# Performance work log

Measured on AMD Instinct MI355X. Metric: run time of the kernel, lower is better.

## Reference

```python
import jax, jax.numpy as jnp
import numpy as np

B, C, T, H = 64, 64, 2048, 128  # batch, input channels, time steps, hidden_dim


def setup_inputs() -> dict:
    key = jax.random.key(0)
    ks = jax.random.split(key, 14)
    s = 0.05
    d = {
        'x': jax.random.normal(ks[0], (B, C, T), jnp.float32),
        # forward-direction LSTM params (PyTorch gate order i,f,g,o)
        'Wih_f': jax.random.normal(ks[1], (4 * H, C), jnp.float32) * s,
        'Whh_f': jax.random.normal(ks[2], (4 * H, H), jnp.float32) * s,
        'bih_f': jax.random.normal(ks[3], (4 * H,), jnp.float32) * s,
        'bhh_f': jax.random.normal(ks[4], (4 * H,), jnp.float32) * s,
        # backward-direction LSTM params
        'Wih_b': jax.random.normal(ks[5], (4 * H, C), jnp.float32) * s,
        'Whh_b': jax.random.normal(ks[6], (4 * H, H), jnp.float32) * s,
        'bih_b': jax.random.normal(ks[7], (4 * H,), jnp.float32) * s,
        'bhh_b': jax.random.normal(ks[8], (4 * H,), jnp.float32) * s,
        # attention params
        'Wa': jax.random.normal(ks[9], (2 * H, 2 * H), jnp.float32) * s,
        'ba': jax.random.normal(ks[10], (2 * H,), jnp.float32) * s,
        'Wu': jax.random.normal(ks[11], (1, 2 * H), jnp.float32) * s,
        'bu': jax.random.normal(ks[12], (1,), jnp.float32) * s,
    }
    return d


def _lstm_dir(xt, Wih, Whh, bih, bhh):
    # xt: (B, T, C) -> hs: (B, T, H). PyTorch gate order: i, f, g, o.
    Bb, Tt, _ = xt.shape
    Hh = Whh.shape[1]
    z_in = jnp.einsum('btc,gc->btg', xt, Wih) + bih + bhh  # (B, T, 4H)

    def step(carry, z_t):
        h, c = carry
        z = z_t + h @ Whh.T
        i, f, g, o = jnp.split(z, 4, axis=-1)
        c = jax.nn.sigmoid(f) * c + jax.nn.sigmoid(i) * jnp.tanh(g)
        h = jax.nn.sigmoid(o) * jnp.tanh(c)
        return (h, c), h

    h0 = jnp.zeros((Bb, Hh), xt.dtype)
    _, hs = jax.lax.scan(step, (h0, h0), jnp.swapaxes(z_in, 0, 1))
    return jnp.swapaxes(hs, 0, 1)


def reference(x, Wih_f, Whh_f, bih_f, bhh_f, Wih_b, Whh_b, bih_b, bhh_b, Wa, ba, Wu, bu):
    xt = jnp.swapaxes(x, 1, 2)                       # (B, T, C)
    h_fwd = _lstm_dir(xt, Wih_f, Whh_f, bih_f, bhh_f)
    h_bwd = _lstm_dir(xt[:, ::-1], Wih_b, Whh_b, bih_b, bhh_b)[:, ::-1]
    lstm_out = jnp.concatenate([h_fwd, h_bwd], axis=-1)  # (B, T, 2H)
    u = jnp.tanh(jnp.einsum('bth,gh->btg', lstm_out, Wa) + ba)
    scores = jnp.einsum('btg,og->bto', u, Wu)[..., 0] + bu[0]  # (B, T)
    w = jax.nn.softmax(scores, axis=1)
    attended = jnp.einsum('bth,bt->bh', lstm_out, w)  # (B, 2H)
    return attended
```

## Files before the change

kernel.cpp:

```cpp
#include <hip/hip_runtime.h>
#include <hip/hip_bf16.h>
#include <cstdint>

#define Bb 64
#define Cc 64
#define Tt 2048
#define Hh 128
#define RING 18
#define HRS 1024
#define XPS 524

typedef __fp16 h2    __attribute__((ext_vector_type(2)));
typedef __fp16 f16x8 __attribute__((ext_vector_type(8)));
typedef float  f32x4 __attribute__((ext_vector_type(4)));

union P8 { uint4 u; f16x8 v; h2 p[4]; __fp16 h[8]; };
union P2 { unsigned int u; h2 p; };

#if __has_builtin(__builtin_amdgcn_exp2f)
#define EXP2F(v) __builtin_amdgcn_exp2f(v)
#else
#define EXP2F(v) __expf(0.69314718056f * (v))
#endif
#define RCPF(v) __builtin_amdgcn_rcpf(v)
#define L2E 1.44269504089f

__device__ __forceinline__ float ftanh(float xx) {
    return 1.0f - 2.0f / (__expf(2.0f * xx) + 1.0f);
}

__device__ __forceinline__ f16x8 cvt8s(float4 a, float4 b, float s) {
    P8 u;
    u.p[0] = __builtin_amdgcn_cvt_pkrtz(a.x * s, a.y * s);
    u.p[1] = __builtin_amdgcn_cvt_pkrtz(a.z * s, a.w * s);
    u.p[2] = __builtin_amdgcn_cvt_pkrtz(b.x * s, b.y * s);
    u.p[3] = __builtin_amdgcn_cvt_pkrtz(b.z * s, b.w * s);
    return u.v;
}

__global__ __launch_bounds__(512, 2) void lstm_kernel(
    const float* __restrict__ x,
    const float* __restrict__ Wih_f, const float* __restrict__ Whh_f,
    const float* __restrict__ bih_f, const float* __restrict__ bhh_f,
    const float* __restrict__ Wih_b, const float* __restrict__ Whh_b,
    const float* __restrict__ bih_b, const float* __restrict__ bhh_b,
    __fp16* __restrict__ y)
{
    const int blk = blockIdx.x;
    const int dir = blk >> 2;
    const int bg  = blk & 3;
    const int tid = threadIdx.x;
    const int w   = tid >> 6;
    const int l   = tid & 63;
    const int col = l & 15;
    const int hi  = l >> 4;

    const float* Wih = dir ? Wih_b : Wih_f;
    const float* Whh = dir ? Whh_b : Whh_f;
    const float* bih = dir ? bih_b : bih_f;
    const float* bhh = dir ? bhh_b : bhh_f;

    f16x8 whA[4][4];
    f16x8 wxA[4][2];
    float bias[4][4];
    float cst[4] = {0.0f, 0.0f, 0.0f, 0.0f};
    #pragma unroll
    for (int m = 0; m < 4; ++m) {
        const float s = (m == 2) ? (2.0f * L2E) : L2E;
        const int rowA = (m << 7) + (w << 4) + col;
        #pragma unroll
        for (int kk = 0; kk < 4; ++kk) {
            const float* p = Whh + (size_t)rowA * 128 + kk * 32 + hi * 8;
            whA[m][kk] = cvt8s(*(const float4*)p, *(const float4*)(p + 4), s);
        }
        #pragma unroll
        for (int kk = 0; kk < 2; ++kk) {
            const float* p = Wih + (size_t)rowA * 64 + kk * 32 + hi * 8;
            wxA[m][kk] = cvt8s(*(const float4*)p, *(const float4*)(p + 4), s);
        }
        #pragma unroll
        for (int r = 0; r < 4; ++r) {
            const int rowC = (m << 7) + (w << 4) + (hi << 2) + r;
            bias[m][r] = (bih[rowC] + bhh[rowC]) * s;
        }
    }

    __shared__ __align__(16) unsigned int lds_hr[RING * HRS];
    __shared__ __align__(16) unsigned int lds_xs[16 * XPS];

    for (int i = tid; i < HRS; i += 512) lds_hr[(RING - 1) * HRS + i] = 0u;

    const int gsw = ((hi << 4) + (col ^ hi)) << 2;
    const int hiw = ((w & 1) << 1) + (hi >> 1);
    const int wgsw = ((w >> 1) << 8) + (((hiw << 4) + (col ^ hiw)) << 2) + ((hi & 1) << 1);

    const size_t xbase = (size_t)(bg * 16) * Cc * Tt;
    int slp = RING - 1;
    int slc = 0;

    #pragma unroll 1
    for (int tile = 0; tile < Tt / 16; ++tile) {
        const int s0  = tile << 4;
        const int sl0 = slc;

        #pragma unroll
        for (int it = 0; it < 4; ++it) {
            int i = tid + (it << 9);
            int tq = i & 3, cp = (i >> 2) & 31, b = i >> 7;
            int tb = dir ? (Tt - 4 - s0 - (tq << 2)) : (s0 + (tq << 2));
            const float* rA = x + xbase + ((size_t)b * Cc + 2 * cp) * Tt + tb;
            float4 va = *(const float4*)rA;
            float4 vb = *(const float4*)(rA + Tt);
            const float* pa = (const float*)&va;
            const float* pb = (const float*)&vb;
            int kk = cp >> 4, hip = (cp >> 2) & 3, e2 = cp & 3;
            int gdst = (kk << 8) + (((hip << 4) + (b ^ hip)) << 2) + e2;
            #pragma unroll
            for (int e = 0; e < 4; ++e) {
                int ss = dir ? ((tq << 2) + 3 - e) : ((tq << 2) + e);
                P2 pk; pk.p = __builtin_amdgcn_cvt_pkrtz(pa[e], pb[e]);
                lds_xs[ss * XPS + gdst] = pk.u;
            }
        }
        __syncthreads();

        #pragma unroll 1
        for (int ss = 0; ss < 16; ++ss) {
            const unsigned int* hbase = lds_hr + slp * HRS;
            const unsigned int* xbase2 = lds_xs + ss * XPS;
            P8 hB[4], xB[2];
            #pragma unroll
            for (int kk = 0; kk < 4; ++kk)
                hB[kk].u = *(const uint4*)(hbase + (kk << 8) + gsw);
            #pragma unroll
            for (int kk = 0; kk < 2; ++kk)
                xB[kk].u = *(const uint4*)(xbase2 + (kk << 8) + gsw);

            f32x4 acc[4];
            #pragma unroll
            for (int m = 0; m < 4; ++m) {
                f32x4 a = {0.0f, 0.0f, 0.0f, 0.0f};
                #pragma unroll
                for (int kk = 0; kk < 4; ++kk)
                    a = __builtin_amdgcn_mfma_f32_16x16x32_f16(whA[m][kk], hB[kk].v, a, 0, 0, 0);
                #pragma unroll
                for (int kk = 0; kk < 2; ++kk)
                    a = __builtin_amdgcn_mfma_f32_16x16x32_f16(wxA[m][kk], xB[kk].v, a, 0, 0, 0);
                acc[m] = a;
            }

            float hhv[4];
            #pragma unroll
            for (int r = 0; r < 4; ++r) {
                float zi = acc[0][r] + bias[0][r];
                float zf = acc[1][r] + bias[1][r];
                float zg = acc[2][r] + bias[2][r];
                float zo = acc[3][r] + bias[3][r];
                float si = RCPF(1.0f + EXP2F(-zi));
                float sf = RCPF(1.0f + EXP2F(-zf));
                float so = RCPF(1.0f + EXP2F(-zo));
                float tg = fmaf(-2.0f, RCPF(1.0f + EXP2F(zg)), 1.0f);
                float c  = fmaf(sf, cst[r], si * tg);
                cst[r] = c;
                float tc = fmaf(-2.0f, RCPF(1.0f + EXP2F(2.0f * L2E * c)), 1.0f);
                hhv[r] = so * tc;
            }
            P2 hp0, hp1;
            hp0.p = __builtin_amdgcn_cvt_pkrtz(hhv[0], hhv[1]);
            hp1.p = __builtin_amdgcn_cvt_pkrtz(hhv[2], hhv[3]);
            uint2 wv; wv.x = hp0.u; wv.y = hp1.u;
            *(uint2*)(lds_hr + slc * HRS + wgsw) = wv;
            __syncthreads();
            slp = slc;
            slc = (slc + 1 == RING) ? 0 : slc + 1;
        }

        #pragma unroll
        for (int it = 0; it < 8; ++it) {
            int idx = (it << 3) + w;
            int ssf = idx >> 2, kkf = idx & 3;
            int sl = sl0 + ssf; if (sl >= RING) sl -= RING;
            uint4 v = *(const uint4*)(lds_hr + sl * HRS + (kkf << 8) + (l << 2));
            int bf = (l & 15) ^ (l >> 4);
            int j8 = (kkf << 2) + (l >> 4);
            int t = dir ? (Tt - 1 - (s0 + ssf)) : (s0 + ssf);
            *(uint4*)(y + (((size_t)(bg * 16 + bf) * Tt + t) << 8) + dir * 128 + (j8 << 3)) = v;
        }
    }
}

__global__ __launch_bounds__(512, 2) void attn_scores_kernel(
    const __fp16* __restrict__ y,
    const float* __restrict__ Wa, const float* __restrict__ ba,
    const float* __restrict__ Wu, const float* __restrict__ bu,
    float* __restrict__ scores)
{
    const int b   = blockIdx.y;
    const int t0  = blockIdx.x * 64;
    const int tid = threadIdx.x;
    const int w   = tid >> 6, l = tid & 63;
    const int col = l & 15, hi = l >> 4;

    __shared__ __fp16 y_lds[64][264];
    __shared__ float red[8][64];

    f16x8 wB[2][8];
    float bav[2], wuv[2];
    #pragma unroll
    for (int ns = 0; ns < 2; ++ns) {
        const int g = (w << 5) + (ns << 4) + col;
        #pragma unroll
        for (int kk = 0; kk < 8; ++kk) {
            const float* p = Wa + (size_t)g * 256 + kk * 32 + hi * 8;
            wB[ns][kk] = cvt8s(*(const float4*)p, *(const float4*)(p + 4), 1.0f);
        }
        bav[ns] = ba[g];
        wuv[ns] = Wu[g];
    }

    #pragma unroll
    for (int it = 0; it < 4; ++it) {
        int i = tid + it * 512;
        int tt = i >> 5, c8 = i & 31;
        uint4 v = *(const uint4*)(y + ((size_t)b * Tt + t0 + tt) * 256 + c8 * 8);
        *(uint4*)&y_lds[tt][c8 * 8] = v;
    }
    __syncthreads();

    f32x4 acc[4][2];
    #pragma unroll
    for (int ms = 0; ms < 4; ++ms)
        #pragma unroll
        for (int ns = 0; ns < 2; ++ns) {
            acc[ms][ns][0] = bav[ns]; acc[ms][ns][1] = bav[ns];
            acc[ms][ns][2] = bav[ns]; acc[ms][ns][3] = bav[ns];
        }

    #pragma unroll
    for (int ms = 0; ms < 4; ++ms) {
        #pragma unroll
        for (int kk = 0; kk < 8; ++kk) {
            P8 a;
            a.u = *(const uint4*)&y_lds[(ms << 4) + col][kk * 32 + hi * 8];
            acc[ms][0] = __builtin_amdgcn_mfma_f32_16x16x32_f16(a.v, wB[0][kk], acc[ms][0], 0, 0, 0);
            acc[ms][1] = __builtin_amdgcn_mfma_f32_16x16x32_f16(a.v, wB[1][kk], acc[ms][1], 0, 0, 0);
        }
    }

    #pragma unroll
    for (int ms = 0; ms < 4; ++ms) {
        float pr[4];
        #pragma unroll
        for (int r = 0; r < 4; ++r) {
            pr[r] = wuv[0] * ftanh(acc[ms][0][r]) + wuv[1] * ftanh(acc[ms][1][r]);
            pr[r] += __shfl_xor(pr[r], 1, 64);
            pr[r] += __shfl_xor(pr[r], 2, 64);
            pr[r] += __shfl_xor(pr[r], 4, 64);
            pr[r] += __shfl_xor(pr[r], 8, 64);
        }
        if (col == 0) {
            #pragma unroll
            for (int r = 0; r < 4; ++r)
                red[w][(ms << 4) + (hi << 2) + r] = pr[r];
        }
    }
    __syncthreads();
    if (tid < 64) {
        float ssum = bu[0];
        #pragma unroll
        for (int wv = 0; wv < 8; ++wv) ssum += red[wv][tid];
        scores[(size_t)b * Tt + t0 + tid] = ssum;
    }
}

__global__ __launch_bounds__(256) void attn_out_kernel(
    const __fp16* __restrict__ y,
    const float* __restrict__ scores,
    float* __restrict__ out)
{
    const int b = blockIdx.x;
    const int tid = threadIdx.x;
    const int lane = tid & 63, wid = tid >> 6;
    __shared__ float wls[2048];
    __shared__ float red[4];

    float m = -1e30f;
    for (int t = tid; t < Tt; t += 256) m = fmaxf(m, scores[(size_t)b * Tt + t]);
    #pragma unroll
    for (int off = 32; off >= 1; off >>= 1) m = fmaxf(m, __shfl_xor(m, off, 64));
    if (lane == 0) red[wid] = m;
    __syncthreads();
    m = fmaxf(fmaxf(red[0], red[1]), fmaxf(red[2], red[3]));
    __syncthreads();

    float sum = 0.0f;
    for (int t = tid; t < Tt; t += 256) {
        float e = __expf(scores[(size_t)b * Tt + t] - m);
        wls[t] = e;
        sum += e;
    }
    #pragma unroll
    for (int off = 32; off >= 1; off >>= 1) sum += __shfl_xor(sum, off, 64);
    if (lane == 0) red[wid] = sum;
    __syncthreads();
    const float inv = 1.0f / (red[0] + red[1] + red[2] + red[3]);

    const __fp16* yb = y + (size_t)b * Tt * 256 + tid;
    float acc = 0.0f;
    for (int t = 0; t < Tt; ++t) {
        acc += wls[t] * (float)yb[(size_t)t * 256];
    }
    out[b * 256 + tid] = acc * inv;
}

extern "C" void kernel_launch(void* const* d_in, const int* in_sizes, int n_in,
                              void* d_out, int out_size, void* d_ws, size_t ws_size,
                              hipStream_t stream) {
    const float* x     = (const float*)d_in[0];
    const float* Wih_f = (const float*)d_in[1];
    const float* Whh_f = (const float*)d_in[2];
    const float* bih_f = (const float*)d_in[3];
    const float* bhh_f = (const float*)d_in[4];
    const float* Wih_b = (const float*)d_in[5];
    const float* Whh_b = (const float*)d_in[6];
    const float* bih_b = (const float*)d_in[7];
    const float* bhh_b = (const float*)d_in[8];
    const float* Wa    = (const float*)d_in[9];
    const float* ba    = (const float*)d_in[10];
    const float* Wu    = (const float*)d_in[11];
    const float* bu    = (const float*)d_in[12];
    float* out = (float*)d_out;

    __fp16* y = (__fp16*)d_ws;
    float* scores = (float*)((char*)d_ws + (size_t)Bb * Tt * 256 * sizeof(__fp16));

    hipLaunchKernelGGL(lstm_kernel, dim3(8), dim3(512), 0, stream,
                       x, Wih_f, Whh_f, bih_f, bhh_f, Wih_b, Whh_b, bih_b, bhh_b, y);
    hipLaunchKernelGGL(attn_scores_kernel, dim3(Tt / 64, Bb), dim3(512), 0, stream,
                       y, Wa, ba, Wu, bu, scores);
    hipLaunchKernelGGL(attn_out_kernel, dim3(Bb), dim3(256), 0, stream, y, scores, out);
}
```

Before: 2.241 ms.

## Precompute next step's input-projection MFMAs off the recurrence critical path

The input-projection MFMAs (Wih·x plus bias) for step ss+1 are now issued during step ss, after the recurrent MFMAs, and their result seeds the accumulator of the next step. This takes the x-projection and the bias adds off the serial h dependency chain. The gate math is also reformulated to merge the sigmoid(i)*tanh(g) and sigmoid(o)*tanh(c) reciprocals into one reciprocal each, cutting transcendental ops. The 16-step inner loop is fully unrolled with double-buffered accumulators, which raises register pressure at 2 blocks per CU.

```diff
diff --git a/kernel.cpp b/kernel.cpp
--- a/kernel.cpp
+++ b/kernel.cpp
@@ -37,6 +37,70 @@
     u.p[3] = __builtin_amdgcn_cvt_pkrtz(b.z * s, b.w * s);
     return u.v;
 }
+
+
+#define XMFMA(DST, SS) do {                                                            \
+    const unsigned int* xr_ = lds_xs + (SS) * XPS;                                     \
+    P8 xb0_, xb1_;                                                                     \
+    xb0_.u = *(const uint4*)(xr_ + gsw);                                               \
+    xb1_.u = *(const uint4*)(xr_ + 256 + gsw);                                         \
+    DST[0] = __builtin_amdgcn_mfma_f32_16x16x32_f16(wxA[0][0], xb0_.v, biasv[0], 0, 0, 0); \
+    DST[1] = __builtin_amdgcn_mfma_f32_16x16x32_f16(wxA[1][0], xb0_.v, biasv[1], 0, 0, 0); \
+    DST[2] = __builtin_amdgcn_mfma_f32_16x16x32_f16(wxA[2][0], xb0_.v, biasv[2], 0, 0, 0); \
+    DST[3] = __builtin_amdgcn_mfma_f32_16x16x32_f16(wxA[3][0], xb0_.v, biasv[3], 0, 0, 0); \
+    DST[0] = __builtin_amdgcn_mfma_f32_16x16x32_f16(wxA[0][1], xb1_.v, DST[0], 0, 0, 0);   \
+    DST[1] = __builtin_amdgcn_mfma_f32_16x16x32_f16(wxA[1][1], xb1_.v, DST[1], 0, 0, 0);   \
+    DST[2] = __builtin_amdgcn_mfma_f32_16x16x32_f16(wxA[2][1], xb1_.v, DST[2], 0, 0, 0);   \
+    DST[3] = __builtin_amdgcn_mfma_f32_16x16x32_f16(wxA[3][1], xb1_.v, DST[3], 0, 0, 0);   \
+} while (0)
+
+#define LSTM_STEP(SS, CUR, NXT, DO_NX) do {                                            \
+    const unsigned int* hbase_ = lds_hr + slp * HRS;                                   \
+    P8 hB0_, hB1_, hB2_, hB3_;                                                         \
+    hB0_.u = *(const uint4*)(hbase_ + 0 * 256 + gsw);                                  \
+    hB1_.u = *(const uint4*)(hbase_ + 1 * 256 + gsw);                                  \
+    hB2_.u = *(const uint4*)(hbase_ + 2 * 256 + gsw);                                  \
+    hB3_.u = *(const uint4*)(hbase_ + 3 * 256 + gsw);                                  \
+    f32x4 a0_ = __builtin_amdgcn_mfma_f32_16x16x32_f16(whA[0][0], hB0_.v, CUR[0], 0, 0, 0); \
+    f32x4 a1_ = __builtin_amdgcn_mfma_f32_16x16x32_f16(whA[1][0], hB0_.v, CUR[1], 0, 0, 0); \
+    f32x4 a2_ = __builtin_amdgcn_mfma_f32_16x16x32_f16(whA[2][0], hB0_.v, CUR[2], 0, 0, 0); \
+    f32x4 a3_ = __builtin_amdgcn_mfma_f32_16x16x32_f16(whA[3][0], hB0_.v, CUR[3], 0, 0, 0); \
+    a0_ = __builtin_amdgcn_mfma_f32_16x16x32_f16(whA[0][1], hB1_.v, a0_, 0, 0, 0);     \
+    a1_ = __builtin_amdgcn_mfma_f32_16x16x32_f16(whA[1][1], hB1_.v, a1_, 0, 0, 0);     \
+    a2_ = __builtin_amdgcn_mfma_f32_16x16x32_f16(whA[2][1], hB1_.v, a2_, 0, 0, 0);     \
+    a3_ = __builtin_amdgcn_mfma_f32_16x16x32_f16(whA[3][1], hB1_.v, a3_, 0, 0, 0);     \
+    a0_ = __builtin_amdgcn_mfma_f32_16x16x32_f16(whA[0][2], hB2_.v, a0_, 0, 0, 0);     \
+    a1_ = __builtin_amdgcn_mfma_f32_16x16x32_f16(whA[1][2], hB2_.v, a1_, 0, 0, 0);     \
+    a2_ = __builtin_amdgcn_mfma_f32_16x16x32_f16(whA[2][2], hB2_.v, a2_, 0, 0, 0);     \
+    a3_ = __builtin_amdgcn_mfma_f32_16x16x32_f16(whA[3][2], hB2_.v, a3_, 0, 0, 0);     \
+    a0_ = __builtin_amdgcn_mfma_f32_16x16x32_f16(whA[0][3], hB3_.v, a0_, 0, 0, 0);     \
+    a1_ = __builtin_amdgcn_mfma_f32_16x16x32_f16(whA[1][3], hB3_.v, a1_, 0, 0, 0);     \
+    a2_ = __builtin_amdgcn_mfma_f32_16x16x32_f16(whA[2][3], hB3_.v, a2_, 0, 0, 0);     \
+    a3_ = __builtin_amdgcn_mfma_f32_16x16x32_f16(whA[3][3], hB3_.v, a3_, 0, 0, 0);     \
+    if (DO_NX) { XMFMA(NXT, (SS) + 1); }                                               \
+    float hhv_[4];                                                                     \
+    _Pragma("unroll")                                                                  \
+    for (int r_ = 0; r_ < 4; ++r_) {                                                   \
+        float zi_ = a0_[r_], zf_ = a1_[r_], zg_ = a2_[r_], zo_ = a3_[r_];              \
+        float ea_ = EXP2F(-zi_);                                                       \
+        float eb_ = EXP2F(-zg_);                                                       \
+        float sf_ = RCPF(1.0f + EXP2F(-zf_));                                          \
+        float sitg_ = (1.0f - eb_) * RCPF((1.0f + ea_) * (1.0f + eb_));                \
+        float c_ = fmaf(sf_, cst[r_], sitg_);                                          \
+        cst[r_] = c_;                                                                  \
+        float ed_ = EXP2F(-((2.0f * L2E) * c_));                                       \
+        float eo_ = EXP2F(-zo_);                                                       \
+        hhv_[r_] = (1.0f - ed_) * RCPF((1.0f + eo_) * (1.0f + ed_));                   \
+    }                                                                                  \
+    P2 q0_, q1_;                                                                       \
+    q0_.p = __builtin_amdgcn_cvt_pkrtz(hhv_[0], hhv_[1]);                              \
+    q1_.p = __builtin_amdgcn_cvt_pkrtz(hhv_[2], hhv_[3]);                              \
+    uint2 wv_; wv_.x = q0_.u; wv_.y = q1_.u;                                           \
+    *(uint2*)(lds_hr + slc * HRS + wgsw) = wv_;                                        \
+    __syncthreads();                                                                   \
+    slp = slc;                                                                         \
+    slc = (slc + 1 == RING) ? 0 : slc + 1;                                             \
+} while (0)
 
 __global__ __launch_bounds__(512, 2) void lstm_kernel(
     const float* __restrict__ x,
@@ -62,7 +126,7 @@
 
     f16x8 whA[4][4];
     f16x8 wxA[4][2];
-    float bias[4][4];
+    f32x4 biasv[4];
     float cst[4] = {0.0f, 0.0f, 0.0f, 0.0f};
     #pragma unroll
     for (int m = 0; m < 4; ++m) {
@@ -81,7 +145,7 @@
         #pragma unroll
         for (int r = 0; r < 4; ++r) {
             const int rowC = (m << 7) + (w << 4) + (hi << 2) + r;
-            bias[m][r] = (bih[rowC] + bhh[rowC]) * s;
+            biasv[m][r] = (bih[rowC] + bhh[rowC]) * s;
         }
     }
 
@@ -97,6 +161,8 @@
     const size_t xbase = (size_t)(bg * 16) * Cc * Tt;
     int slp = RING - 1;
     int slc = 0;
+
+    f32x4 xaccA[4], xaccB[4];
 
     #pragma unroll 1
     for (int tile = 0; tile < Tt / 16; ++tile) {
@@ -124,55 +190,12 @@
         }
         __syncthreads();
 
-        #pragma unroll 1
-        for (int ss = 0; ss < 16; ++ss) {
-            const unsigned int* hbase = lds_hr + slp * HRS;
-            const unsigned int* xbase2 = lds_xs + ss * XPS;
-            P8 hB[4], xB[2];
-            #pragma unroll
-            for (int kk = 0; kk < 4; ++kk)
-                hB[kk].u = *(const uint4*)(hbase + (kk << 8) + gsw);
-            #pragma unroll
-            for (int kk = 0; kk < 2; ++kk)
-                xB[kk].u = *(const uint4*)(xbase2 + (kk << 8) + gsw);
-
-            f32x4 acc[4];
-            #pragma unroll
-            for (int m = 0; m < 4; ++m) {
-                f32x4 a = {0.0f, 0.0f, 0.0f, 0.0f};
-                #pragma unroll
-                for (int kk = 0; kk < 4; ++kk)
-                    a = __builtin_amdgcn_mfma_f32_16x16x32_f16(whA[m][kk], hB[kk].v, a, 0, 0, 0);
-                #pragma unroll
-                for (int kk = 0; kk < 2; ++kk)
-                    a = __builtin_amdgcn_mfma_f32_16x16x32_f16(wxA[m][kk], xB[kk].v, a, 0, 0, 0);
-                acc[m] = a;
-            }
-
-            float hhv[4];
-            #pragma unroll
-            for (int r = 0; r < 4; ++r) {
-                float zi = acc[0][r] + bias[0][r];
-                float zf = acc[1][r] + bias[1][r];
-                float zg = acc[2][r] + bias[2][r];
-                float zo = acc[3][r] + bias[3][r];
-                float si = RCPF(1.0f + EXP2F(-zi));
-                float sf = RCPF(1.0f + EXP2F(-zf));
-                float so = RCPF(1.0f + EXP2F(-zo));
-                float tg = fmaf(-2.0f, RCPF(1.0f + EXP2F(zg)), 1.0f);
-                float c  = fmaf(sf, cst[r], si * tg);
-                cst[r] = c;
-                float tc = fmaf(-2.0f, RCPF(1.0f + EXP2F(2.0f * L2E * c)), 1.0f);
-                hhv[r] = so * tc;
-            }
-            P2 hp0, hp1;
-            hp0.p = __builtin_amdgcn_cvt_pkrtz(hhv[0], hhv[1]);
-            hp1.p = __builtin_amdgcn_cvt_pkrtz(hhv[2], hhv[3]);
-            uint2 wv; wv.x = hp0.u; wv.y = hp1.u;
-            *(uint2*)(lds_hr + slc * HRS + wgsw) = wv;
-            __syncthreads();
-            slp = slc;
-            slc = (slc + 1 == RING) ? 0 : slc + 1;
+        XMFMA(xaccA, 0);
+
+        #pragma unroll
+        for (int ss = 0; ss < 16; ss += 2) {
+            LSTM_STEP(ss,     xaccA, xaccB, true);
+            LSTM_STEP(ss + 1, xaccB, xaccA, (ss + 1) < 15);
         }
 
         #pragma unroll
```

After: 2.133 ms. 4.9% less time.
